# Kernel tuning notes

Hardware: AMD Instinct MI355X
Metric: run time of the kernel (lower is better)

## Reference

```python
import jax, jax.numpy as jnp
import numpy as np

B, C, N, L = 64, 32, 500, 12
C_OUT = 32
C_CAT = 9 * C  # (order*(support_len+1)+1)*c_in = 288


def setup_inputs() -> dict:
    key = jax.random.key(0)
    ks = jax.random.split(key, 7)
    x = jax.random.normal(ks[0], (B, C, N, L), dtype=jnp.float32)
    # row-stochastic-ish adjacencies: scale by 1/N to keep hops numerically tame
    A0 = jax.random.uniform(ks[1], (N, N), dtype=jnp.float32) / N
    A1 = jax.random.uniform(ks[2], (N, N), dtype=jnp.float32) / N
    A2 = jax.random.uniform(ks[3], (N, N), dtype=jnp.float32) / N
    A3 = jax.random.uniform(ks[4], (B, N, N), dtype=jnp.float32) / N
    W = jax.random.normal(ks[5], (C_OUT, C_CAT), dtype=jnp.float32) * 0.05
    b = jax.random.normal(ks[6], (C_OUT,), dtype=jnp.float32) * 0.05
    return {"x": x, "A0": A0, "A1": A1, "A2": A2, "A3": A3, "W": W, "b": b}


def reference(x, A0, A1, A2, A3, W, b):
    # x: [B, C, N, L]; A0..A2: [N, N]; A3: [B, N, N]; W: [C_OUT, 9*C]; b: [C_OUT]
    def hop2(h, A):  # static adjacency
        return jnp.einsum('ncvl,vw->ncwl', h, A)

    def hop3(h, A):  # batched (dynamic) adjacency
        return jnp.einsum('ncvl,nvw->ncwl', h, A)

    out = [x]
    for A in (A0, A1, A2):
        x1 = hop2(x, A)
        x2 = hop2(x1, A)
        out.extend([x1, x2])
    x1 = hop3(x, A3)
    x2 = hop3(x1, A3)
    out.extend([x1, x2])

    h = jnp.concatenate(out, axis=1)  # [B, 9C, N, L]
    # 1x1 Conv2d == channel mixing matmul + bias
    h = jnp.einsum('ncvl,oc->novl', h, W) + b[None, :, None, None]
    # dropout in eval mode: identity
    return h
```

## Files before the change

kernel.cpp:

```cpp
#include <hip/hip_runtime.h>

typedef unsigned short u16;
typedef __bf16 bf16x8 __attribute__((ext_vector_type(8)));
typedef float f32x4 __attribute__((ext_vector_type(4)));
typedef const unsigned int __attribute__((address_space(1))) gu32;
typedef unsigned int __attribute__((address_space(3))) lu32;

#define NN 500
#define LLc 12
#define CC 32
#define MM 384
#define KP 512
#define MT 96
#define NT2 128
#define XS_S 40
#define AS_S 40
#define CT2_S 136
#define TS_S 384
#define AT_ELS 256000

__device__ __forceinline__ u16 f2bf(float f) {
    union { float f; unsigned u; } cv; cv.f = f;
    unsigned u = cv.u;
    u += 0x7fffu + ((u >> 16) & 1u);
    return (u16)(u >> 16);
}
__device__ __forceinline__ float bf2f(u16 s) {
    union { unsigned u; float f; } cv; cv.u = ((unsigned)s) << 16;
    return cv.f;
}

__global__ __launch_bounds__(256) void prep_all(
    const float* __restrict__ x,
    const float* __restrict__ A0, const float* __restrict__ A1,
    const float* __restrict__ A2, const float* __restrict__ A3,
    u16* __restrict__ At_s, u16* __restrict__ At_b,
    u16* __restrict__ Xt,
    const float* __restrict__ W, u16* __restrict__ Wp)
{
    __shared__ u16 Ls[MM * 36];
    const int id = blockIdx.x;
    const int t = threadIdx.x;

    if (id < 17152) {
        int rem = id & 255;
        int z  = id >> 8;
        int n0 = (rem & 15) * 32;
        int k0 = (rem >> 4) * 32;
        const float* Ab; u16* Ob;
        if (z == 0)      { Ab = A0; Ob = At_s; }
        else if (z == 1) { Ab = A1; Ob = At_s + (long)AT_ELS; }
        else if (z == 2) { Ab = A2; Ob = At_s + 2L * AT_ELS; }
        else             { Ab = A3 + (long)(z - 3) * NN * NN; Ob = At_b + (long)(z - 3) * AT_ELS; }
        {
            int vl = t >> 3, u = t & 7;
            float4 v = make_float4(0.f, 0.f, 0.f, 0.f);
            if (k0 + vl < NN && n0 + 4 * u + 4 <= NN)
                v = *(const float4*)(Ab + (long)(k0 + vl) * NN + n0 + 4 * u);
            int nb = 4 * u;
            Ls[(nb + 0) * 36 + vl] = f2bf(v.x);
            Ls[(nb + 1) * 36 + vl] = f2bf(v.y);
            Ls[(nb + 2) * 36 + vl] = f2bf(v.z);
            Ls[(nb + 3) * 36 + vl] = f2bf(v.w);
        }
        __syncthreads();
        {
            int row = t >> 3, u = t & 7;
            if (n0 + row < NN)
                *(uint2*)(Ob + (long)(n0 + row) * KP + k0 + 4 * u) = *(const uint2*)(&Ls[row * 36 + 4 * u]);
        }
    } else if (id < 18176) {
        int jj = id - 17152;
        int v0 = (jj & 15) * 32;
        int b  = jj >> 4;
        #pragma unroll
        for (int j = 0; j < 12; ++j) {
            int f = t + 256 * j;
            int c = f / 96;
            int r = f - c * 96;
            int vl = r / 3;
            int l3 = (r - vl * 3) * 4;
            float4 v = make_float4(0.f, 0.f, 0.f, 0.f);
            if (v0 + vl < NN)
                v = *(const float4*)(x + ((long)b * CC + c) * (NN * LLc) + (long)(v0 + vl) * LLc + l3);
            int mb = (c * LLc + l3) * 36 + vl;
            Ls[mb]       = f2bf(v.x);
            Ls[mb + 36]  = f2bf(v.y);
            Ls[mb + 72]  = f2bf(v.z);
            Ls[mb + 108] = f2bf(v.w);
        }
        __syncthreads();
        #pragma unroll
        for (int j = 0; j < 12; ++j) {
            int f = t + 256 * j;
            int row = f >> 3, u = f & 7;
            *(uint2*)(Xt + ((long)b * MM + row) * KP + v0 + 4 * u) = *(const uint2*)(&Ls[row * 36 + 4 * u]);
        }
    } else {
        int idx = (id - 18176) * 256 + t;
        int j    = idx & 7;
        int lane = (idx >> 3) & 63;
        int p    = (idx >> 9) & 1;
        int mt   = (idx >> 10) & 1;
        int g    = idx >> 11;
        int o  = mt * 16 + (lane & 15);
        int kk = g * 32 + (lane >> 4) * 8 + j;
        float wv = W[o * 288 + kk];
        u16 hi = f2bf(wv);
        Wp[idx] = (p == 0) ? hi : f2bf(wv - bf2f(hi));
    }
}

__global__ __launch_bounds__(256) void atrans_all(
    const float* __restrict__ A0, const float* __restrict__ A1,
    const float* __restrict__ A2, const float* __restrict__ A3,
    u16* __restrict__ At_s, u16* __restrict__ At_b)
{
    __shared__ u16 Ls[32 * 36];
    const int t = threadIdx.x;
    const int n0 = blockIdx.x * 32;
    const int k0 = blockIdx.y * 32;
    const int z = blockIdx.z;
    const float* Ab; u16* Ob;
    if (z == 0)      { Ab = A0; Ob = At_s; }
    else if (z == 1) { Ab = A1; Ob = At_s + (long)AT_ELS; }
    else if (z == 2) { Ab = A2; Ob = At_s + 2L * AT_ELS; }
    else             { Ab = A3 + (long)(z - 3) * NN * NN; Ob = At_b + (long)(z - 3) * AT_ELS; }
    {
        int vl = t >> 3, u = t & 7;
        float4 v = make_float4(0.f, 0.f, 0.f, 0.f);
        if (k0 + vl < NN && n0 + 4 * u + 4 <= NN)
            v = *(const float4*)(Ab + (long)(k0 + vl) * NN + n0 + 4 * u);
        int nb = 4 * u;
        Ls[(nb + 0) * 36 + vl] = f2bf(v.x);
        Ls[(nb + 1) * 36 + vl] = f2bf(v.y);
        Ls[(nb + 2) * 36 + vl] = f2bf(v.z);
        Ls[(nb + 3) * 36 + vl] = f2bf(v.w);
    }
    __syncthreads();
    {
        int row = t >> 3, u = t & 7;
        if (n0 + row < NN)
            *(uint2*)(Ob + (long)(n0 + row) * KP + k0 + 4 * u) = *(const uint2*)(&Ls[row * 36 + 4 * u]);
    }
}

__global__ __launch_bounds__(256) void xpose_kernel(
    const float* __restrict__ x, u16* __restrict__ Xt)
{
    __shared__ u16 Ls[MM * 36];
    const int t = threadIdx.x;
    const int v0 = blockIdx.x * 32;
    const int b  = blockIdx.y;
    #pragma unroll
    for (int j = 0; j < 12; ++j) {
        int f = t + 256 * j;
        int c = f / 96;
        int r = f - c * 96;
        int vl = r / 3;
        int l3 = (r - vl * 3) * 4;
        float4 v = make_float4(0.f, 0.f, 0.f, 0.f);
        if (v0 + vl < NN)
            v = *(const float4*)(x + ((long)b * CC + c) * (NN * LLc) + (long)(v0 + vl) * LLc + l3);
        int mb = (c * LLc + l3) * 36 + vl;
        Ls[mb]       = f2bf(v.x);
        Ls[mb + 36]  = f2bf(v.y);
        Ls[mb + 72]  = f2bf(v.z);
        Ls[mb + 108] = f2bf(v.w);
    }
    __syncthreads();
    #pragma unroll
    for (int j = 0; j < 12; ++j) {
        int f = t + 256 * j;
        int row = f >> 3, u = f & 7;
        *(uint2*)(Xt + ((long)b * MM + row) * KP + v0 + 4 * u) = *(const uint2*)(&Ls[row * 36 + 4 * u]);
    }
}

__global__ __launch_bounds__(256) void wpack_kernel(
    const float* __restrict__ W, u16* __restrict__ Wp)
{
    int idx = blockIdx.x * 256 + threadIdx.x;
    int j    = idx & 7;
    int lane = (idx >> 3) & 63;
    int p    = (idx >> 9) & 1;
    int mt   = (idx >> 10) & 1;
    int g    = idx >> 11;
    int o  = mt * 16 + (lane & 15);
    int kk = g * 32 + (lane >> 4) * 8 + j;
    float wv = W[o * 288 + kk];
    u16 hi = f2bf(wv);
    Wp[idx] = (p == 0) ? hi : f2bf(wv - bf2f(hi));
}

__global__ __launch_bounds__(256, 3) void hop_fast7(
    const u16* __restrict__ Xsrc, long x_gstride, long x_bstride,
    const u16* __restrict__ At_s,
    const u16* __restrict__ At_b,
    u16* __restrict__ Hout, long h_gstride)
{
    __shared__ __align__(16) u16 smem[24576];
    u16* Ct = smem;

    const int t = threadIdx.x;
    const int lane = t & 63;
    const int wv = t >> 6;
    const int f0 = blockIdx.x + 4 * (blockIdx.y + 3 * blockIdx.z);
    const int w  = (f0 & 7) * 384 + (f0 >> 3);
    const int zc = w / 12;
    const int rem = w - zc * 12;
    const int bx = rem & 3;
    const int by = rem >> 2;
    const int g  = zc & 3;
    const int b  = zc >> 2;
    const int n0 = bx * 128;
    const int m0 = by * 128;
    const int ln  = lane & 15;
    const int q16 = lane >> 4;

    const u16* Ab = (g < 3) ? (At_s + (long)g * AT_ELS) : (At_b + (long)b * AT_ELS);
    const u16* Xb = Xsrc + (long)g * x_gstride + (long)b * x_bstride;
    u16* Ob = Hout + (long)g * h_gstride + (long)b * ((long)MM * KP);

    const int rbase = lane >> 2;
    const int coff  = (((lane & 3) ^ ((lane >> 3) & 3)) << 3);
    const int rsel  = ((q16 ^ ((ln >> 1) & 3)) << 3);

    auto STAGE = [&](int kk, int pb) {
        #pragma unroll
        for (int j = 0; j < 4; ++j) {
            int o = (wv * 4 + j) << 10;
            const u16* src;
            if (o < 8192) {
                src = Ab + (long)(n0 + (o >> 6) + rbase) * KP + kk + coff;
            } else {
                src = Xb + (long)(m0 + (o >> 6) - 128 + rbase) * KP + kk + coff;
            }
            __builtin_amdgcn_global_load_lds((gu32*)src,
                (lu32*)((char*)smem + pb * 16384 + o), 16, 0, 0);
        }
    };

    f32x4 acc[2][8];
    #pragma unroll
    for (int ns = 0; ns < 2; ++ns)
        #pragma unroll
        for (int i = 0; i < 8; ++i)
            #pragma unroll
            for (int r = 0; r < 4; ++r) acc[ns][i][r] = 0.f;

    auto COMPUTE = [&](int pb) {
        const u16* As = smem + pb * 8192;
        const u16* Xs = As + 4096;
        bf16x8 b0 = *(const bf16x8*)(&As[(wv * 32 + ln) * 32 + rsel]);
        bf16x8 b1 = *(const bf16x8*)(&As[(wv * 32 + 16 + ln) * 32 + rsel]);
        __builtin_amdgcn_s_setprio(1);
        #pragma unroll
        for (int i = 0; i < 8; ++i) {
            bf16x8 af = *(const bf16x8*)(&Xs[(i * 16 + ln) * 32 + rsel]);
            acc[0][i] = __builtin_amdgcn_mfma_f32_16x16x32_bf16(af, b0, acc[0][i], 0, 0, 0);
            acc[1][i] = __builtin_amdgcn_mfma_f32_16x16x32_bf16(af, b1, acc[1][i], 0, 0, 0);
        }
        __builtin_amdgcn_s_setprio(0);
    };

    STAGE(0, 0);
    STAGE(32, 1);
    int c0 = 0, c1 = 1, c2 = 2;
    #pragma unroll 1
    for (int s = 0; s < 15; ++s) {
        asm volatile("s_waitcnt vmcnt(4)" ::: "memory");
        __builtin_amdgcn_s_barrier();
        __builtin_amdgcn_sched_barrier(0);
        if (s <= 13) STAGE(32 * (s + 2), c2);
        COMPUTE(c0);
        int tmp = c0; c0 = c1; c1 = c2; c2 = tmp;
    }
    asm volatile("s_waitcnt vmcnt(0)" ::: "memory");
    __builtin_amdgcn_s_barrier();
    __builtin_amdgcn_sched_barrier(0);
    COMPUTE(c0);

    #pragma unroll
    for (int h = 0; h < 2; ++h) {
        __syncthreads();
        #pragma unroll
        for (int ns = 0; ns < 2; ++ns) {
            int col = wv * 32 + ns * 16 + ln;
            #pragma unroll
            for (int i4 = 0; i4 < 4; ++i4) {
                int rb = i4 * 16 + (lane >> 4) * 4;
                #pragma unroll
                for (int r = 0; r < 4; ++r)
                    Ct[(rb + r) * CT2_S + col] = f2bf(acc[ns][h * 4 + i4][r]);
            }
        }
        __syncthreads();
        #pragma unroll
        for (int j = 0; j < 8; ++j) {
            int f = t + 256 * j;
            int row = f >> 5, u = f & 31;
            int n = n0 + 4 * u;
            uint2 v = make_uint2(0u, 0u);
            if (n < NN) v = *(const uint2*)(&Ct[row * CT2_S + 4 * u]);
            *(uint2*)(Ob + (long)(m0 + h * 64 + row) * KP + n) = v;
        }
    }
}

__global__ __launch_bounds__(256, 3) void hop_fast3(
    const u16* __restrict__ Xsrc, long x_gstride, long x_bstride, int x_rstride, int x_klim,
    const u16* __restrict__ At_s,
    const u16* __restrict__ At_b,
    u16* __restrict__ Hout, long h_gstride)
{
    __shared__ __align__(16) u16 smem[13056];
    u16* As = smem;
    u16* Xs = smem + 5120;
    u16* Ct = smem;

    const int t = threadIdx.x;
    const int lane = t & 63;
    const int wv = t >> 6;
    const int f0 = blockIdx.x + 4 * blockIdx.y + 8 * blockIdx.z;
    const int w  = (f0 & 7) * 256 + (f0 >> 3);
    const int bx = w & 3;
    const int by = (w >> 2) & 1;
    const int zc = w >> 3;
    const int g  = zc & 3;
    const int b  = zc >> 2;
    const int n0 = bx * NT2;
    const int m0 = by * 192;
    const int ln = lane & 15;
    const int q8 = (lane >> 4) * 8;

    const u16* Ab = (g < 3) ? (At_s + (long)g * AT_ELS) : (At_b + (long)b * AT_ELS);
    const u16* Xb = Xsrc + (long)g * x_gstride + (long)b * x_bstride;
    u16* Ob = Hout + (long)g * h_gstride + (long)b * ((long)MM * NN);

    uint2 pa[4], px[6];
    auto loadA = [&](int k0) {
        #pragma unroll
        for (int j = 0; j < 4; ++j) {
            int f = t + 256 * j;
            int n = f >> 3, u = f & 7;
            uint2 v = make_uint2(0u, 0u);
            if (n0 + n < NN)
                v = *(const uint2*)(Ab + (long)(n0 + n) * KP + k0 + 4 * u);
            pa[j] = v;
        }
    };
    auto loadX = [&](int k0) {
        #pragma unroll
        for (int j = 0; j < 6; ++j) {
            int f = t + 256 * j;
            int r = f >> 3, u = f & 7;
            int k = k0 + 4 * u;
            uint2 v = make_uint2(0u, 0u);
            if (k < x_klim)
                v = *(const uint2*)(Xb + (long)(m0 + r) * x_rstride + k);
            px[j] = v;
        }
    };

    f32x4 acc[2][12];
    #pragma unroll
    for (int ns = 0; ns < 2; ++ns)
        #pragma unroll
        for (int i = 0; i < 12; ++i)
            #pragma unroll
            for (int r = 0; r < 4; ++r) acc[ns][i][r] = 0.f;

    loadA(0);
    loadX(0);
    #pragma unroll 1
    for (int s = 0; s < 16; ++s) {
        __syncthreads();
        #pragma unroll
        for (int j = 0; j < 4; ++j) {
            int f = t + 256 * j;
            *(uint2*)(&As[(f >> 3) * AS_S + 4 * (f & 7)]) = pa[j];
        }
        #pragma unroll
        for (int j = 0; j < 6; ++j) {
            int f = t + 256 * j;
            *(uint2*)(&Xs[(f >> 3) * XS_S + 4 * (f & 7)]) = px[j];
        }
        if (s < 15) {
            loadA(32 * (s + 1));
            loadX(32 * (s + 1));
        }
        __syncthreads();
        bf16x8 b0 = *(const bf16x8*)(&As[(wv * 32 + ln) * AS_S + q8]);
        bf16x8 b1 = *(const bf16x8*)(&As[(wv * 32 + 16 + ln) * AS_S + q8]);
        #pragma unroll
        for (int i = 0; i < 12; ++i) {
            bf16x8 af = *(const bf16x8*)(&Xs[(i * 16 + ln) * XS_S + q8]);
            acc[0][i] = __builtin_amdgcn_mfma_f32_16x16x32_bf16(af, b0, acc[0][i], 0, 0, 0);
            acc[1][i] = __builtin_amdgcn_mfma_f32_16x16x32_bf16(af, b1, acc[1][i], 0, 0, 0);
        }
    }

    #pragma unroll
    for (int h = 0; h < 2; ++h) {
        __syncthreads();
        #pragma unroll
        for (int ns = 0; ns < 2; ++ns) {
            int col = wv * 32 + ns * 16 + ln;
            #pragma unroll
            for (int i6 = 0; i6 < 6; ++i6) {
                int rb = i6 * 16 + (lane >> 4) * 4;
                #pragma unroll
                for (int r = 0; r < 4; ++r)
                    Ct[(rb + r) * CT2_S + col] = f2bf(acc[ns][h * 6 + i6][r]);
            }
        }
        __syncthreads();
        #pragma unroll
        for (int j = 0; j < 12; ++j) {
            int f = t + 256 * j;
            int row = f >> 5, u = f & 31;
            int n = n0 + 4 * u;
            if (n < NN)
                *(uint2*)(Ob + (long)(m0 + h * 96 + row) * NN + n) = *(const uint2*)(&Ct[row * CT2_S + 4 * u]);
        }
    }
}

__global__ __launch_bounds__(512, 4) void mix_mfma(
    const u16* __restrict__ Xt,
    const u16* __restrict__ H,
    const u16* __restrict__ Wp,
    const float* __restrict__ bias,
    float* __restrict__ out,
    long h_gs, long h_bs, int h_rs)
{
    __shared__ __align__(16) char smem[50176];
    u16*   Ls = (u16*)smem;
    float* Ct = (float*)smem;

    const int t   = threadIdx.x;
    const int wg  = blockIdx.y * 8 + blockIdx.x;
    const int swz = (wg & 7) * 64 + (wg >> 3);
    const int bx  = swz & 7;
    const int b   = swz >> 3;
    const int n0  = bx * 64;
    const int w    = t >> 6;
    const int lane = t & 63;
    const int kq   = lane >> 4;
    const int ln   = lane & 15;
    const int srow   = lane >> 3;
    const int schunk = (lane & 7) * 8;

    f32x4 acc[6][2];
    #pragma unroll
    for (int i = 0; i < 6; ++i)
        #pragma unroll
        for (int m = 0; m < 2; ++m)
            #pragma unroll
            for (int r = 0; r < 4; ++r) acc[i][m][r] = 0.f;

    #pragma unroll 1
    for (int g = 0; g < 9; ++g) {
        const u16* base; int rs;
        if (g == 0) { base = Xt + (long)b * (MM * KP); rs = KP; }
        else {
            int gg = g - 1;
            int buf = (gg & 1) ? 4 + (gg >> 1) : (gg >> 1);
            base = H + (long)buf * h_gs + (long)b * h_bs; rs = h_rs;
        }
        __syncthreads();
        #pragma unroll
        for (int i = 0; i < 6; ++i) {
            int r0 = (w * 6 + i) * 8;
            const u16* src = base + (long)(r0 + srow) * rs + n0 + schunk;
            __builtin_amdgcn_global_load_lds((gu32*)src, (lu32*)(Ls + r0 * 64), 16, 0, 0);
        }
        asm volatile("s_waitcnt vmcnt(0)" ::: "memory");
        __syncthreads();
        uint4 wf[2][2];
        #pragma unroll
        for (int mt = 0; mt < 2; ++mt)
            #pragma unroll
            for (int p = 0; p < 2; ++p)
                wf[mt][p] = *(const uint4*)(Wp + ((((g * 2 + mt) * 2 + p) * 64 + lane) * 8));
        #pragma unroll
        for (int i = 0; i < 6; ++i) {
            int ct = w * 6 + i;
            int off0 = kq * 6144 + (ct >> 2) * 64 + (ct & 3) * 16 + ln;
            union { u16 s[8]; bf16x8 v; } fb;
            #pragma unroll
            for (int j = 0; j < 8; ++j) fb.s[j] = Ls[off0 + j * 768];
            #pragma unroll
            for (int mt = 0; mt < 2; ++mt) {
                acc[i][mt] = __builtin_amdgcn_mfma_f32_16x16x32_bf16(*(const bf16x8*)&wf[mt][0], fb.v, acc[i][mt], 0, 0, 0);
                acc[i][mt] = __builtin_amdgcn_mfma_f32_16x16x32_bf16(*(const bf16x8*)&wf[mt][1], fb.v, acc[i][mt], 0, 0, 0);
            }
        }
    }

    #pragma unroll
    for (int mt = 0; mt < 2; ++mt) {
        __syncthreads();
        #pragma unroll
        for (int i = 0; i < 6; ++i) {
            int col = (w * 6 + i) * 16 + ln;
            #pragma unroll
            for (int r = 0; r < 4; ++r)
                Ct[(kq * 4 + r) * 781 + col] = acc[i][mt][r];
        }
        __syncthreads();
        int o16 = t >> 5, u = t & 31;
        int og = mt * 16 + o16;
        float bs = bias[og];
        float* ob = out + (((long)b * CC + og) * NN + n0) * 12L;
        #pragma unroll
        for (int j2 = 0; j2 < 2; ++j2) {
            int n = u + 32 * j2;
            if (n0 + n < NN) {
                float v[12];
                #pragma unroll
                for (int l = 0; l < 12; ++l) v[l] = Ct[o16 * 781 + l * 64 + n] + bs;
                #pragma unroll
                for (int q = 0; q < 3; ++q)
                    *(float4*)(ob + (long)n * 12 + q * 4) = *(const float4*)&v[q * 4];
            }
        }
    }
}

__global__ __launch_bounds__(256, 3) void mix_all(
    const u16* __restrict__ Xt,
    const u16* __restrict__ H,
    const float* __restrict__ W,
    const float* __restrict__ bias,
    float* __restrict__ out)
{
    __shared__ __align__(16) float smem[96 * 36 + 288 * 33];
    float* ts = smem;
    float* Ws = smem + 96 * 36;

    const int t  = threadIdx.x;
    const int b  = blockIdx.y;
    const int w0 = blockIdx.x * 32;
    const int o  = t & 31;
    const int wq = t >> 5;
    const int w4 = wq * 4;
    const long HBUF = (long)64 * MM * NN;

    #pragma unroll
    for (int j = 0; j < 36; ++j) {
        int f = t + 256 * j;
        int oo = f & 31, ci = f >> 5;
        Ws[ci * 33 + oo] = W[oo * 288 + ci];
    }

    float acc[4][12];
    #pragma unroll
    for (int k = 0; k < 4; ++k)
        #pragma unroll
        for (int l = 0; l < 12; ++l) acc[k][l] = 0.f;

    uint2 px[3];
    auto loadq = [&](int q) {
        int g = q >> 2, c0 = (q & 3) << 3;
        const u16* base; int rs;
        if (g == 0) { base = Xt + (long)b * (MM * KP); rs = KP; }
        else {
            int gg = g - 1, i = gg >> 1;
            int buf = (gg & 1) ? 4 + i : i;
            base = H + (long)buf * HBUF + (long)b * ((long)MM * NN); rs = NN;
        }
        int m0c = c0 * 12;
        #pragma unroll
        for (int j = 0; j < 3; ++j) {
            int f = t + 256 * j;
            int r = f >> 3, u = f & 7;
            px[j] = *(const uint2*)(base + (long)(m0c + r) * rs + w0 + 4 * u);
        }
    };

    loadq(0);
    #pragma unroll 1
    for (int q = 0; q < 36; ++q) {
        __syncthreads();
        #pragma unroll
        for (int j = 0; j < 3; ++j) {
            int f = t + 256 * j;
            int r = f >> 3, u = f & 7;
            uint2 raw = px[j];
            float4 v = make_float4(bf2f((u16)(raw.x & 0xffffu)), bf2f((u16)(raw.x >> 16)),
                                   bf2f((u16)(raw.y & 0xffffu)), bf2f((u16)(raw.y >> 16)));
            *(float4*)(&ts[r * 36 + 4 * u]) = v;
        }
        if (q < 35) loadq(q + 1);
        __syncthreads();
        int g = q >> 2, c0 = (q & 3) << 3;
        #pragma unroll 1
        for (int cl = 0; cl < 8; ++cl) {
            float wgt = Ws[(g * 32 + c0 + cl) * 33 + o];
            #pragma unroll
            for (int l = 0; l < 12; ++l) {
                float4 h = *(const float4*)(&ts[(cl * 12 + l) * 36 + w4]);
                acc[0][l] += wgt * h.x;
                acc[1][l] += wgt * h.y;
                acc[2][l] += wgt * h.z;
                acc[3][l] += wgt * h.w;
            }
        }
    }

    #pragma unroll 1
    for (int r = 0; r < 4; ++r) {
        __syncthreads();
        if ((o >> 3) == r) {
            int ol = o & 7;
            #pragma unroll
            for (int k = 0; k < 4; ++k)
                #pragma unroll
                for (int l = 0; l < 12; ++l)
                    ts[ol * 388 + (w4 + k) * 12 + l] = acc[k][l];
        }
        __syncthreads();
        #pragma unroll
        for (int j = 0; j < 3; ++j) {
            int f4 = t + 256 * j;
            int ol = f4 / 96;
            int rem = f4 - ol * 96;
            int w  = rem / 3;
            int lq = rem - w * 3;
            if (w0 + w < NN) {
                float4 v = *(const float4*)(&ts[ol * 388 + w * 12 + lq * 4]);
                float bs = bias[r * 8 + ol];
                v.x += bs; v.y += bs; v.z += bs; v.w += bs;
                *(float4*)(out + (((long)b * CC + r * 8 + ol) * NN + w0 + w) * LLc + lq * 4) = v;
            }
        }
    }
}

__global__ __launch_bounds__(256, 4) void hop_fast(
    const u16* __restrict__ Xsrc, long x_bstride, int x_rstride, int x_klim,
    const u16* __restrict__ At,   long a_bstride,
    u16* __restrict__ hout)
{
    __shared__ __align__(16) u16 smem[13056];
    u16* As = smem;
    u16* Xs = smem + 5120;
    u16* Ct = smem;

    const int t = threadIdx.x;
    const int lane = t & 63;
    const int wv = t >> 6;
    const int n0 = blockIdx.x * NT2;
    const int m0 = blockIdx.y * MT;
    const int b  = blockIdx.z;
    const int ln = lane & 15;
    const int q8 = (lane >> 4) * 8;

    const u16* Ab = At + (long)b * a_bstride;
    const u16* Xb = Xsrc + (long)b * x_bstride;

    uint2 pa[4], px[3];
    auto loadA = [&](int k0) {
        #pragma unroll
        for (int j = 0; j < 4; ++j) {
            int f = t + 256 * j;
            int n = f >> 3, u = f & 7;
            uint2 v = make_uint2(0u, 0u);
            if (n0 + n < NN)
                v = *(const uint2*)(Ab + (long)(n0 + n) * KP + k0 + 4 * u);
            pa[j] = v;
        }
    };
    auto loadX = [&](int k0) {
        #pragma unroll
        for (int j = 0; j < 3; ++j) {
            int f = t + 256 * j;
            int r = f >> 3, u = f & 7;
            int k = k0 + 4 * u;
            uint2 v = make_uint2(0u, 0u);
            if (k < x_klim)
                v = *(const uint2*)(Xb + (long)(m0 + r) * x_rstride + k);
            px[j] = v;
        }
    };

    f32x4 acc[2][6];
    #pragma unroll
    for (int ns = 0; ns < 2; ++ns)
        #pragma unroll
        for (int i = 0; i < 6; ++i)
            #pragma unroll
            for (int r = 0; r < 4; ++r) acc[ns][i][r] = 0.f;

    loadA(0);
    loadX(0);
    #pragma unroll 1
    for (int s = 0; s < 16; ++s) {
        __syncthreads();
        #pragma unroll
        for (int j = 0; j < 4; ++j) {
            int f = t + 256 * j;
            *(uint2*)(&As[(f >> 3) * AS_S + 4 * (f & 7)]) = pa[j];
        }
        #pragma unroll
        for (int j = 0; j < 3; ++j) {
            int f = t + 256 * j;
            *(uint2*)(&Xs[(f >> 3) * XS_S + 4 * (f & 7)]) = px[j];
        }
        if (s < 15) {
            loadA(32 * (s + 1));
            loadX(32 * (s + 1));
        }
        __syncthreads();
        bf16x8 af[6];
        #pragma unroll
        for (int i = 0; i < 6; ++i)
            af[i] = *(const bf16x8*)(&Xs[(i * 16 + ln) * XS_S + q8]);
        #pragma unroll
        for (int ns = 0; ns < 2; ++ns) {
            bf16x8 bfr = *(const bf16x8*)(&As[(wv * 32 + ns * 16 + ln) * AS_S + q8]);
            #pragma unroll
            for (int i = 0; i < 6; ++i)
                acc[ns][i] = __builtin_amdgcn_mfma_f32_16x16x32_bf16(af[i], bfr, acc[ns][i], 0, 0, 0);
        }
    }

    __syncthreads();
    #pragma unroll
    for (int ns = 0; ns < 2; ++ns) {
        int col = wv * 32 + ns * 16 + ln;
        #pragma unroll
        for (int i = 0; i < 6; ++i) {
            int rb = i * 16 + (lane >> 4) * 4;
            #pragma unroll
            for (int r = 0; r < 4; ++r)
                Ct[(rb + r) * CT2_S + col] = f2bf(acc[ns][i][r]);
        }
    }
    __syncthreads();
    u16* Ob = hout + (long)b * ((long)MM * NN);
    #pragma unroll
    for (int j = 0; j < 12; ++j) {
        int f = t + 256 * j;
        int row = f >> 5, u = f & 31;
        int n = n0 + 4 * u;
        if (n < NN)
            *(uint2*)(Ob + (long)(m0 + row) * NN + n) = *(const uint2*)(&Ct[row * CT2_S + 4 * u]);
    }
}

__global__ __launch_bounds__(256, 2) void mix_kernel(
    const float* __restrict__ x,
    const u16* __restrict__ h1,
    const u16* __restrict__ h2,
    const float* __restrict__ W,
    const float* __restrict__ bias,
    int blk1, int blk2,
    float* __restrict__ out, int init)
{
    __shared__ __align__(16) float smem[CC * TS_S + 3 * 1056];
    float* ts = smem;
    float* Ws = smem + CC * TS_S;

    const int t = threadIdx.x;
    const int b = blockIdx.y;
    const int w0 = blockIdx.x * 32;
    const int o  = t & 15;
    const int wg = (t >> 4) & 7;
    const int lh = t >> 7;

    #pragma unroll
    for (int j = 0; j < 4; ++j) {
        int f = t + 256 * j;
        int oo = f & 31, c = f >> 5;
        Ws[c * 33 + oo]        = W[oo * 288 + blk1 * 32 + c];
        Ws[1056 + c * 33 + oo] = W[oo * 288 + blk2 * 32 + c];
        if (init) Ws[2112 + c * 33 + oo] = W[oo * 288 + c];
    }

    float acc2[2][4][6];
    #pragma unroll
    for (int a = 0; a < 2; ++a)
        #pragma unroll
        for (int q = 0; q < 4; ++q)
            #pragma unroll
            for (int l = 0; l < 6; ++l) acc2[a][q][l] = 0.f;

    auto stage_h = [&](const u16* h) {
        #pragma unroll
        for (int j = 0; j < 12; ++j) {
            int f = t + 256 * j;
            int row = f >> 3, u = f & 7;
            int w = w0 + 4 * u;
            uint2 raw = make_uint2(0u, 0u);
            if (w < NN)
                raw = *(const uint2*)(h + ((long)b * MM + row) * NN + w);
            int c = row / 12;
            int l = row - c * 12;
            float* dst = &ts[c * TS_S + l * 32 + 4 * u];
            dst[0] = bf2f((u16)(raw.x & 0xffffu));
            dst[1] = bf2f((u16)(raw.x >> 16));
            dst[2] = bf2f((u16)(raw.y & 0xffffu));
            dst[3] = bf2f((u16)(raw.y >> 16));
        }
    };
    auto accum = [&](const float* Wg) {
        for (int c = 0; c < CC; ++c) {
            float w1 = Wg[c * 33 + o];
            float w2 = Wg[c * 33 + o + 16];
            #pragma unroll
            for (int l6 = 0; l6 < 6; ++l6) {
                const float4 hv = *(const float4*)(&ts[c * TS_S + (lh * 6 + l6) * 32 + wg * 4]);
                acc2[0][0][l6] += w1 * hv.x;
                acc2[0][1][l6] += w1 * hv.y;
                acc2[0][2][l6] += w1 * hv.z;
                acc2[0][3][l6] += w1 * hv.w;
                acc2[1][0][l6] += w2 * hv.x;
                acc2[1][1][l6] += w2 * hv.y;
                acc2[1][2][l6] += w2 * hv.z;
                acc2[1][3][l6] += w2 * hv.w;
            }
        }
    };

    if (init) {
        #pragma unroll
        for (int j = 0; j < 12; ++j) {
            int f = t + 256 * j;
            int c = f / 96;
            int r = f - c * 96;
            int w = r / 3;
            int q = r - w * 3;
            float4 v = make_float4(0.f, 0.f, 0.f, 0.f);
            if (w0 + w < NN)
                v = *(const float4*)(x + ((long)b * CC + c) * (NN * LLc) + (long)(w0 + w) * LLc + q * 4);
            float* dst = &ts[c * TS_S + (q * 4) * 32 + w];
            dst[0]  = v.x; dst[32] = v.y; dst[64] = v.z; dst[96] = v.w;
        }
        __syncthreads();
        accum(Ws + 2112);
        __syncthreads();
    }
    stage_h(h1);
    __syncthreads();
    accum(Ws);
    __syncthreads();
    stage_h(h2);
    __syncthreads();
    accum(Ws + 1056);

    #pragma unroll
    for (int oh = 0; oh < 2; ++oh) {
        int oo = o + 16 * oh;
        float bs = init ? bias[oo] : 0.f;
        #pragma unroll
        for (int q = 0; q < 4; ++q) {
            int w = w0 + wg * 4 + q;
            if (w < NN) {
                float* op = out + ((long)b * CC + oo) * (NN * LLc) + (long)w * LLc + lh * 6;
                #pragma unroll
                for (int p = 0; p < 3; ++p) {
                    float2* pp = (float2*)op + p;
                    float2 v;
                    if (init) {
                        v.x = bs + acc2[oh][q][2 * p];
                        v.y = bs + acc2[oh][q][2 * p + 1];
                    } else {
                        v = *pp;
                        v.x += acc2[oh][q][2 * p];
                        v.y += acc2[oh][q][2 * p + 1];
                    }
                    *pp = v;
                }
            }
        }
    }
}

extern "C" void kernel_launch(void* const* d_in, const int* in_sizes, int n_in,
                              void* d_out, int out_size, void* d_ws, size_t ws_size,
                              hipStream_t stream) {
    const float* x    = (const float*)d_in[0];
    const float* A0   = (const float*)d_in[1];
    const float* A1   = (const float*)d_in[2];
    const float* A2   = (const float*)d_in[3];
    const float* A3   = (const float*)d_in[4];
    const float* W    = (const float*)d_in[5];
    const float* bias = (const float*)d_in[6];
    float* out = (float*)d_out;
    char* ws = (char*)d_ws;

    const size_t HBUF_ELS  = (size_t)64 * MM * NN;
    const size_t H8_BYTES  = 8 * HBUF_ELS * 2;
    const size_t AT_BYTES  = (size_t)AT_ELS * 2;
    const size_t A3T_BYTES = 64 * AT_BYTES;
    const size_t XT_BYTES  = (size_t)64 * MM * KP * 2;
    const size_t need2 = H8_BYTES + 3 * AT_BYTES + A3T_BYTES + XT_BYTES;
    const size_t WPK_BYTES = 36864;
    const size_t need3 = need2 + WPK_BYTES;
    const size_t HB2_ELS  = (size_t)64 * MM * KP;
    const size_t H8B_PAD  = 8 * HB2_ELS * 2;
    const size_t need4 = H8B_PAD + 3 * AT_BYTES + A3T_BYTES + XT_BYTES + WPK_BYTES;

    dim3 blk(256);

    if (ws_size >= need4) {
        u16* Hb   = (u16*)ws;
        u16* At_s = (u16*)(ws + H8B_PAD);
        u16* A3t  = At_s + 3L * AT_ELS;
        u16* Xt   = (u16*)(ws + H8B_PAD + 3 * AT_BYTES + A3T_BYTES);
        u16* Wpk  = Xt + (size_t)64 * MM * KP;

        prep_all<<<dim3(18248), blk, 0, stream>>>(x, A0, A1, A2, A3, At_s, A3t, Xt, W, Wpk);
        hop_fast7<<<dim3(4, 3, 256), blk, 0, stream>>>(
            Xt, 0L, (long)MM * KP, At_s, A3t, Hb, (long)HB2_ELS);
        hop_fast7<<<dim3(4, 3, 256), blk, 0, stream>>>(
            Hb, (long)HB2_ELS, (long)MM * KP, At_s, A3t,
            Hb + 4 * HB2_ELS, (long)HB2_ELS);
        mix_mfma<<<dim3(8, 64), dim3(512), 0, stream>>>(
            Xt, Hb, Wpk, bias, out, (long)HB2_ELS, (long)MM * KP, KP);
        return;
    }

    dim3 hgrid(4, 2, 256);

    if (ws_size >= need3) {
        u16* Hb   = (u16*)ws;
        u16* At_s = (u16*)(ws + H8_BYTES);
        u16* A3t  = At_s + 3L * AT_ELS;
        u16* Xt   = (u16*)(ws + H8_BYTES + 3 * AT_BYTES + A3T_BYTES);
        u16* Wpk  = (u16*)(ws + need2);

        atrans_all<<<dim3(16, 16, 67), blk, 0, stream>>>(A0, A1, A2, A3, At_s, A3t);
        xpose_kernel<<<dim3(16, 64), blk, 0, stream>>>(x, Xt);
        wpack_kernel<<<dim3(72), blk, 0, stream>>>(W, Wpk);
        hop_fast3<<<hgrid, blk, 0, stream>>>(
            Xt, 0L, (long)MM * KP, KP, KP, At_s, A3t, Hb, (long)HBUF_ELS);
        hop_fast3<<<hgrid, blk, 0, stream>>>(
            Hb, (long)HBUF_ELS, (long)MM * NN, NN, NN, At_s, A3t,
            Hb + 4 * HBUF_ELS, (long)HBUF_ELS);
        mix_mfma<<<dim3(8, 64), dim3(512), 0, stream>>>(
            Xt, Hb, Wpk, bias, out, (long)HBUF_ELS, (long)MM * NN, NN);
        return;
    }

    if (ws_size >= need2) {
        u16* H    = (u16*)ws;
        u16* At_s = (u16*)(ws + H8_BYTES);
        u16* A3t  = At_s + 3L * AT_ELS;
        u16* Xt   = (u16*)(ws + H8_BYTES + 3 * AT_BYTES + A3T_BYTES);

        atrans_all<<<dim3(16, 16, 67), blk, 0, stream>>>(A0, A1, A2, A3, At_s, A3t);
        xpose_kernel<<<dim3(16, 64), blk, 0, stream>>>(x, Xt);
        hop_fast3<<<hgrid, blk, 0, stream>>>(
            Xt, 0L, (long)MM * KP, KP, KP, At_s, A3t, H, (long)HBUF_ELS);
        hop_fast3<<<hgrid, blk, 0, stream>>>(
            H, (long)HBUF_ELS, (long)MM * NN, NN, NN, At_s, A3t,
            H + 4 * HBUF_ELS, (long)HBUF_ELS);
        mix_all<<<dim3(16, 64), blk, 0, stream>>>(Xt, H, W, bias, out);
        return;
    }

    const size_t H_BYTES   = HBUF_ELS * 2;
    const size_t need_at   = 2 * H_BYTES + 3 * AT_BYTES + A3T_BYTES;

    u16* H1 = (u16*)ws;
    u16* H2 = (u16*)(ws + H_BYTES);
    u16* At0 = (u16*)(ws + 2 * H_BYTES);
    u16* A3t = At0 + 3L * AT_ELS;
    u16* Xt  = (u16*)(ws + need_at);

    dim3 fgrid(4, 4, 64);
    dim3 mgrid(16, 64);

    xpose_kernel<<<dim3(16, 64), blk, 0, stream>>>(x, Xt);
    atrans_all<<<dim3(16, 16, 67), blk, 0, stream>>>(A0, A1, A2, A3, At0, A3t);

    const long XT_BS = (long)MM * KP;
    const long H_BS  = (long)MM * NN;
    u16* Atp[4] = {At0, At0 + (long)AT_ELS, At0 + 2L * AT_ELS, A3t};

    for (int i = 0; i < 4; ++i) {
        long a_bs = (i == 3) ? (long)AT_ELS : 0;
        hop_fast<<<fgrid, blk, 0, stream>>>(Xt, XT_BS, KP, KP, Atp[i], a_bs, H1);
        hop_fast<<<fgrid, blk, 0, stream>>>(H1, H_BS, NN, NN, Atp[i], a_bs, H2);
        mix_kernel<<<mgrid, blk, 0, stream>>>(i == 0 ? x : nullptr, H1, H2, W, bias,
                                              2 * i + 1, 2 * i + 2, out, i == 0 ? 1 : 0);
    }
}
```

Before: 364.4 us.

## Emit hop outputs in mix-friendly channel-contiguous layout and stream mix from global

Adds a new path in which the hop kernels write their results twice: in the existing K-major layout for the second hop, and in an (l, n, c)-contiguous layout grouped by 8 channels that the mix kernel can read directly as MFMA B fragments. The hop tile changes to 96 rows (8 channels × 12 timesteps) so each block owns whole channel groups. The second hop skips the K-major write entirely. mix_stream drops LDS staging and the scalar gather transposes, loading 16-byte fragments straight from global. The cost is extra writes and workspace in the first hop, and a different hop tiling.

Measured after the change: 365.7 us. About the same (+0.4%).

```diff
diff --git a/kernel.cpp b/kernel.cpp
--- a/kernel.cpp
+++ b/kernel.cpp
@@ -18,6 +18,10 @@
 #define CT2_S 136
 #define TS_S 384
 #define AT_ELS 256000
+#define HM_G 12288000L
+#define HM_B 192000L
+#define HCL_G 12582912L
+#define HCL_B 196608L
 
 __device__ __forceinline__ u16 f2bf(float f) {
     union { float f; unsigned u; } cv; cv.f = f;
@@ -35,7 +39,7 @@
     const float* __restrict__ A0, const float* __restrict__ A1,
     const float* __restrict__ A2, const float* __restrict__ A3,
     u16* __restrict__ At_s, u16* __restrict__ At_b,
-    u16* __restrict__ Xt,
+    u16* __restrict__ Xt, u16* __restrict__ Xm,
     const float* __restrict__ W, u16* __restrict__ Wp)
 {
     __shared__ u16 Ls[MM * 36];
@@ -96,6 +100,24 @@
             int row = f >> 3, u = f & 7;
             *(uint2*)(Xt + ((long)b * MM + row) * KP + v0 + 4 * u) = *(const uint2*)(&Ls[row * 36 + 4 * u]);
         }
+        if (Xm) {
+            u16* Xb = Xm + (long)b * HM_B;
+            #pragma unroll
+            for (int j = 0; j < 6; ++j) {
+                int f = t + 256 * j;
+                int vl = f & 31;
+                int lq = f >> 5;
+                int l  = lq % 12;
+                int cq = lq / 12;
+                if (v0 + vl < NN) {
+                    union { u16 s[8]; uint4 v; } pk;
+                    #pragma unroll
+                    for (int c8 = 0; c8 < 8; ++c8)
+                        pk.s[c8] = Ls[((cq * 8 + c8) * 12 + l) * 36 + vl];
+                    *(uint4*)(Xb + ((long)(l * NN + v0 + vl)) * 32 + cq * 8) = pk.v;
+                }
+            }
+        }
     } else {
         int idx = (id - 18176) * 256 + t;
         int j    = idx & 7;
@@ -108,6 +130,446 @@
         float wv = W[o * 288 + kk];
         u16 hi = f2bf(wv);
         Wp[idx] = (p == 0) ? hi : f2bf(wv - bf2f(hi));
+    }
+}
+
+__global__ __launch_bounds__(256, 3) void hop_fast8(
+    const u16* __restrict__ Xsrc, long x_gstride, long x_bstride,
+    const u16* __restrict__ At_s,
+    const u16* __restrict__ At_b,
+    u16* __restrict__ Hcl,
+    u16* __restrict__ HmArg)
+{
+    __shared__ __align__(16) u16 smem[21504];
+    u16* Ct = smem;
+
+    const int t = threadIdx.x;
+    const int lane = t & 63;
+    const int wv = t >> 6;
+    const int f0 = blockIdx.x + 4 * (blockIdx.y + 4 * blockIdx.z);
+    const int w  = (f0 & 7) * 2048 + (f0 >> 3);
+    const int zc = w >> 4;
+    const int rem = w & 15;
+    const int bx = rem & 3;
+    const int my = rem >> 2;
+    const int g  = zc & 3;
+    const int b  = zc >> 2;
+    const int n0 = bx * NT2;
+    const int m0 = my * 96;
+    const int cb = my * 8;
+    const int ln  = lane & 15;
+    const int q16 = lane >> 4;
+
+    const u16* Ab = (g < 3) ? (At_s + (long)g * AT_ELS) : (At_b + (long)b * AT_ELS);
+    const u16* Xb = Xsrc + (long)g * x_gstride + (long)b * x_bstride;
+
+    const int rbase = lane >> 2;
+    const int coff  = (((lane & 3) ^ ((lane >> 3) & 3)) << 3);
+    const int rsel  = ((q16 ^ ((ln >> 1) & 3)) << 3);
+
+    auto STAGE = [&](int kk, int pb) {
+        char* base = (char*)smem + pb * 14336;
+        if (wv < 2) {
+            #pragma unroll
+            for (int j = 0; j < 4; ++j) {
+                int r16 = wv * 4 + j;
+                const u16* src = Ab + (long)(n0 + r16 * 16 + rbase) * KP + kk + coff;
+                __builtin_amdgcn_global_load_lds((gu32*)src, (lu32*)(base + r16 * 1024), 16, 0, 0);
+            }
+        } else {
+            #pragma unroll
+            for (int j = 0; j < 3; ++j) {
+                int r16 = (wv - 2) * 3 + j;
+                const u16* src = Xb + (long)(m0 + r16 * 16 + rbase) * KP + kk + coff;
+                __builtin_amdgcn_global_load_lds((gu32*)src, (lu32*)(base + 8192 + r16 * 1024), 16, 0, 0);
+            }
+        }
+    };
+
+    f32x4 acc[2][6];
+    #pragma unroll
+    for (int ns = 0; ns < 2; ++ns)
+        #pragma unroll
+        for (int i = 0; i < 6; ++i)
+            #pragma unroll
+            for (int r = 0; r < 4; ++r) acc[ns][i][r] = 0.f;
+
+    auto COMPUTE = [&](int pb) {
+        const u16* As = smem + pb * 7168;
+        const u16* Xs = As + 4096;
+        bf16x8 b0 = *(const bf16x8*)(&As[(wv * 32 + ln) * 32 + rsel]);
+        bf16x8 b1 = *(const bf16x8*)(&As[(wv * 32 + 16 + ln) * 32 + rsel]);
+        __builtin_amdgcn_s_setprio(1);
+        #pragma unroll
+        for (int i = 0; i < 6; ++i) {
+            bf16x8 af = *(const bf16x8*)(&Xs[(i * 16 + ln) * 32 + rsel]);
+            acc[0][i] = __builtin_amdgcn_mfma_f32_16x16x32_bf16(af, b0, acc[0][i], 0, 0, 0);
+            acc[1][i] = __builtin_amdgcn_mfma_f32_16x16x32_bf16(af, b1, acc[1][i], 0, 0, 0);
+        }
+        __builtin_amdgcn_s_setprio(0);
+    };
+
+    STAGE(0, 0);
+    STAGE(32, 1);
+    int c0 = 0, c1 = 1, c2 = 2;
+    #pragma unroll 1
+    for (int s = 0; s < 15; ++s) {
+        if (wv < 2) asm volatile("s_waitcnt vmcnt(4)" ::: "memory");
+        else        asm volatile("s_waitcnt vmcnt(3)" ::: "memory");
+        __builtin_amdgcn_s_barrier();
+        __builtin_amdgcn_sched_barrier(0);
+        if (s <= 13) STAGE(32 * (s + 2), c2);
+        COMPUTE(c0);
+        int tmp = c0; c0 = c1; c1 = c2; c2 = tmp;
+    }
+    asm volatile("s_waitcnt vmcnt(0)" ::: "memory");
+    __builtin_amdgcn_s_barrier();
+    __builtin_amdgcn_sched_barrier(0);
+    COMPUTE(c0);
+
+    __syncthreads();
+    #pragma unroll
+    for (int ns = 0; ns < 2; ++ns) {
+        int col = wv * 32 + ns * 16 + ln;
+        #pragma unroll
+        for (int i6 = 0; i6 < 6; ++i6) {
+            int rb = i6 * 16 + (lane >> 4) * 4;
+            #pragma unroll
+            for (int r = 0; r < 4; ++r)
+                Ct[(rb + r) * CT2_S + col] = f2bf(acc[ns][i6][r]);
+        }
+    }
+    __syncthreads();
+    if (Hcl) {
+        u16* Ocl = Hcl + (long)g * HCL_G + (long)b * HCL_B;
+        #pragma unroll
+        for (int j = 0; j < 12; ++j) {
+            int f = t + 256 * j;
+            int row = f >> 5, u = f & 31;
+            int n = n0 + 4 * u;
+            uint2 v = make_uint2(0u, 0u);
+            if (n < NN) v = *(const uint2*)(&Ct[row * CT2_S + 4 * u]);
+            *(uint2*)(Ocl + (long)(m0 + row) * KP + n) = v;
+        }
+    }
+    {
+        u16* Om = HmArg + (long)g * HM_G + (long)b * HM_B;
+        #pragma unroll
+        for (int j = 0; j < 6; ++j) {
+            int f = t + 256 * j;
+            int n_l = f & 127;
+            int l   = f >> 7;
+            int n = n0 + n_l;
+            if (n < NN) {
+                union { u16 s[8]; uint4 v; } pk;
+                #pragma unroll
+                for (int c8 = 0; c8 < 8; ++c8)
+                    pk.s[c8] = Ct[(c8 * 12 + l) * CT2_S + n_l];
+                *(uint4*)(Om + ((long)(l * NN + n)) * 32 + cb) = pk.v;
+            }
+        }
+    }
+}
+
+__global__ __launch_bounds__(256, 3) void hop_fast7(
+    const u16* __restrict__ Xsrc, long x_gstride, long x_bstride,
+    const u16* __restrict__ At_s,
+    const u16* __restrict__ At_b,
+    u16* __restrict__ Hout, long h_gstride)
+{
+    __shared__ __align__(16) u16 smem[24576];
+    u16* Ct = smem;
+
+    const int t = threadIdx.x;
+    const int lane = t & 63;
+    const int wv = t >> 6;
+    const int f0 = blockIdx.x + 4 * (blockIdx.y + 3 * blockIdx.z);
+    const int w  = (f0 & 7) * 384 + (f0 >> 3);
+    const int zc = w / 12;
+    const int rem = w - zc * 12;
+    const int bx = rem & 3;
+    const int by = rem >> 2;
+    const int g  = zc & 3;
+    const int b  = zc >> 2;
+    const int n0 = bx * 128;
+    const int m0 = by * 128;
+    const int ln  = lane & 15;
+    const int q16 = lane >> 4;
+
+    const u16* Ab = (g < 3) ? (At_s + (long)g * AT_ELS) : (At_b + (long)b * AT_ELS);
+    const u16* Xb = Xsrc + (long)g * x_gstride + (long)b * x_bstride;
+    u16* Ob = Hout + (long)g * h_gstride + (long)b * ((long)MM * KP);
+
+    const int rbase = lane >> 2;
+    const int coff  = (((lane & 3) ^ ((lane >> 3) & 3)) << 3);
+    const int rsel  = ((q16 ^ ((ln >> 1) & 3)) << 3);
+
+    auto STAGE = [&](int kk, int pb) {
+        #pragma unroll
+        for (int j = 0; j < 4; ++j) {
+            int o = (wv * 4 + j) << 10;
+            const u16* src;
+            if (o < 8192) src = Ab + (long)(n0 + (o >> 6) + rbase) * KP + kk + coff;
+            else          src = Xb + (long)(m0 + (o >> 6) - 128 + rbase) * KP + kk + coff;
+            __builtin_amdgcn_global_load_lds((gu32*)src,
+                (lu32*)((char*)smem + pb * 16384 + o), 16, 0, 0);
+        }
+    };
+
+    f32x4 acc[2][8];
+    #pragma unroll
+    for (int ns = 0; ns < 2; ++ns)
+        #pragma unroll
+        for (int i = 0; i < 8; ++i)
+            #pragma unroll
+            for (int r = 0; r < 4; ++r) acc[ns][i][r] = 0.f;
+
+    auto COMPUTE = [&](int pb) {
+        const u16* As = smem + pb * 8192;
+        const u16* Xs = As + 4096;
+        bf16x8 b0 = *(const bf16x8*)(&As[(wv * 32 + ln) * 32 + rsel]);
+        bf16x8 b1 = *(const bf16x8*)(&As[(wv * 32 + 16 + ln) * 32 + rsel]);
+        __builtin_amdgcn_s_setprio(1);
+        #pragma unroll
+        for (int i = 0; i < 8; ++i) {
+            bf16x8 af = *(const bf16x8*)(&Xs[(i * 16 + ln) * 32 + rsel]);
+            acc[0][i] = __builtin_amdgcn_mfma_f32_16x16x32_bf16(af, b0, acc[0][i], 0, 0, 0);
+            acc[1][i] = __builtin_amdgcn_mfma_f32_16x16x32_bf16(af, b1, acc[1][i], 0, 0, 0);
+        }
+        __builtin_amdgcn_s_setprio(0);
+    };
+
+    STAGE(0, 0);
+    STAGE(32, 1);
+    int c0 = 0, c1 = 1, c2 = 2;
+    #pragma unroll 1
+    for (int s = 0; s < 15; ++s) {
+        asm volatile("s_waitcnt vmcnt(4)" ::: "memory");
+        __builtin_amdgcn_s_barrier();
+        __builtin_amdgcn_sched_barrier(0);
+        if (s <= 13) STAGE(32 * (s + 2), c2);
+        COMPUTE(c0);
+        int tmp = c0; c0 = c1; c1 = c2; c2 = tmp;
+    }
+    asm volatile("s_waitcnt vmcnt(0)" ::: "memory");
+    __builtin_amdgcn_s_barrier();
+    __builtin_amdgcn_sched_barrier(0);
+    COMPUTE(c0);
+
+    #pragma unroll
+    for (int h = 0; h < 2; ++h) {
+        __syncthreads();
+        #pragma unroll
+        for (int ns = 0; ns < 2; ++ns) {
+            int col = wv * 32 + ns * 16 + ln;
+            #pragma unroll
+            for (int i4 = 0; i4 < 4; ++i4) {
+                int rb = i4 * 16 + (lane >> 4) * 4;
+                #pragma unroll
+                for (int r = 0; r < 4; ++r)
+                    Ct[(rb + r) * CT2_S + col] = f2bf(acc[ns][h * 4 + i4][r]);
+            }
+        }
+        __syncthreads();
+        #pragma unroll
+        for (int j = 0; j < 8; ++j) {
+            int f = t + 256 * j;
+            int row = f >> 5, u = f & 31;
+            int n = n0 + 4 * u;
+            uint2 v = make_uint2(0u, 0u);
+            if (n < NN) v = *(const uint2*)(&Ct[row * CT2_S + 4 * u]);
+            *(uint2*)(Ob + (long)(m0 + h * 64 + row) * KP + n) = v;
+        }
+    }
+}
+
+__global__ __launch_bounds__(512, 4) void mix_stream(
+    const u16* __restrict__ Xm,
+    const u16* __restrict__ Hm,
+    const u16* __restrict__ Wp,
+    const float* __restrict__ bias,
+    float* __restrict__ out)
+{
+    __shared__ __align__(16) float Ct[12496];
+
+    const int t   = threadIdx.x;
+    const int wg  = blockIdx.y * 8 + blockIdx.x;
+    const int swz = (wg & 7) * 64 + (wg >> 3);
+    const int bx  = swz & 7;
+    const int b   = swz >> 3;
+    const int n0  = bx * 64;
+    const int w    = t >> 6;
+    const int lane = t & 63;
+    const int kq   = lane >> 4;
+    const int ln   = lane & 15;
+
+    f32x4 acc[6][2];
+    #pragma unroll
+    for (int i = 0; i < 6; ++i)
+        #pragma unroll
+        for (int m = 0; m < 2; ++m)
+            #pragma unroll
+            for (int r = 0; r < 4; ++r) acc[i][m][r] = 0.f;
+
+    #pragma unroll 1
+    for (int g = 0; g < 9; ++g) {
+        const u16* src;
+        if (g == 0) src = Xm + (long)b * HM_B;
+        else {
+            int gg = g - 1;
+            int buf = (gg & 1) ? 4 + (gg >> 1) : (gg >> 1);
+            src = Hm + (long)buf * HM_G + (long)b * HM_B;
+        }
+        uint4 wf[2][2];
+        #pragma unroll
+        for (int mt = 0; mt < 2; ++mt)
+            #pragma unroll
+            for (int p = 0; p < 2; ++p)
+                wf[mt][p] = *(const uint4*)(Wp + ((((g * 2 + mt) * 2 + p) * 64 + lane) * 8));
+        #pragma unroll
+        for (int i = 0; i < 6; ++i) {
+            int ct = w * 6 + i;
+            int l  = ct >> 2;
+            int n  = n0 + ((ct & 3) << 4) + ln;
+            uint4 fbv = make_uint4(0u, 0u, 0u, 0u);
+            if (n < NN) fbv = *(const uint4*)(src + ((long)(l * NN + n)) * 32 + kq * 8);
+            bf16x8 fb = *(const bf16x8*)&fbv;
+            acc[i][0] = __builtin_amdgcn_mfma_f32_16x16x32_bf16(*(const bf16x8*)&wf[0][0], fb, acc[i][0], 0, 0, 0);
+            acc[i][0] = __builtin_amdgcn_mfma_f32_16x16x32_bf16(*(const bf16x8*)&wf[0][1], fb, acc[i][0], 0, 0, 0);
+            acc[i][1] = __builtin_amdgcn_mfma_f32_16x16x32_bf16(*(const bf16x8*)&wf[1][0], fb, acc[i][1], 0, 0, 0);
+            acc[i][1] = __builtin_amdgcn_mfma_f32_16x16x32_bf16(*(const bf16x8*)&wf[1][1], fb, acc[i][1], 0, 0, 0);
+        }
+    }
+
+    #pragma unroll
+    for (int mt = 0; mt < 2; ++mt) {
+        __syncthreads();
+        #pragma unroll
+        for (int i = 0; i < 6; ++i) {
+            int col = (w * 6 + i) * 16 + ln;
+            #pragma unroll
+            for (int r = 0; r < 4; ++r)
+                Ct[(kq * 4 + r) * 781 + col] = acc[i][mt][r];
+        }
+        __syncthreads();
+        int o16 = t >> 5, u = t & 31;
+        int og = mt * 16 + o16;
+        float bs = bias[og];
+        float* ob = out + (((long)b * CC + og) * NN + n0) * 12L;
+        #pragma unroll
+        for (int j2 = 0; j2 < 2; ++j2) {
+            int n = u + 32 * j2;
+            if (n0 + n < NN) {
+                float v[12];
+                #pragma unroll
+                for (int l = 0; l < 12; ++l) v[l] = Ct[o16 * 781 + l * 64 + n] + bs;
+                #pragma unroll
+                for (int q = 0; q < 3; ++q)
+                    *(float4*)(ob + (long)n * 12 + q * 4) = *(const float4*)&v[q * 4];
+            }
+        }
+    }
+}
+
+__global__ __launch_bounds__(512, 4) void mix_mfma(
+    const u16* __restrict__ Xt,
+    const u16* __restrict__ H,
+    const u16* __restrict__ Wp,
+    const float* __restrict__ bias,
+    float* __restrict__ out,
+    long h_gs, long h_bs, int h_rs)
+{
+    __shared__ __align__(16) char smem[50176];
+    u16*   Ls = (u16*)smem;
+    float* Ct = (float*)smem;
+
+    const int t   = threadIdx.x;
+    const int wg  = blockIdx.y * 8 + blockIdx.x;
+    const int swz = (wg & 7) * 64 + (wg >> 3);
+    const int bx  = swz & 7;
+    const int b   = swz >> 3;
+    const int n0  = bx * 64;
+    const int w    = t >> 6;
+    const int lane = t & 63;
+    const int kq   = lane >> 4;
+    const int ln   = lane & 15;
+    const int srow   = lane >> 3;
+    const int schunk = (lane & 7) * 8;
+
+    f32x4 acc[6][2];
+    #pragma unroll
+    for (int i = 0; i < 6; ++i)
+        #pragma unroll
+        for (int m = 0; m < 2; ++m)
+            #pragma unroll
+            for (int r = 0; r < 4; ++r) acc[i][m][r] = 0.f;
+
+    #pragma unroll 1
+    for (int g = 0; g < 9; ++g) {
+        const u16* base; int rs;
+        if (g == 0) { base = Xt + (long)b * (MM * KP); rs = KP; }
+        else {
+            int gg = g - 1;
+            int buf = (gg & 1) ? 4 + (gg >> 1) : (gg >> 1);
+            base = H + (long)buf * h_gs + (long)b * h_bs; rs = h_rs;
+        }
+        __syncthreads();
+        #pragma unroll
+        for (int i = 0; i < 6; ++i) {
+            int r0 = (w * 6 + i) * 8;
+            const u16* src = base + (long)(r0 + srow) * rs + n0 + schunk;
+            __builtin_amdgcn_global_load_lds((gu32*)src, (lu32*)(Ls + r0 * 64), 16, 0, 0);
+        }
+        asm volatile("s_waitcnt vmcnt(0)" ::: "memory");
+        __syncthreads();
+        uint4 wf[2][2];
+        #pragma unroll
+        for (int mt = 0; mt < 2; ++mt)
+            #pragma unroll
+            for (int p = 0; p < 2; ++p)
+                wf[mt][p] = *(const uint4*)(Wp + ((((g * 2 + mt) * 2 + p) * 64 + lane) * 8));
+        #pragma unroll
+        for (int i = 0; i < 6; ++i) {
+            int ct = w * 6 + i;
+            int off0 = kq * 6144 + (ct >> 2) * 64 + (ct & 3) * 16 + ln;
+            union { u16 s[8]; bf16x8 v; } fb;
+            #pragma unroll
+            for (int j = 0; j < 8; ++j) fb.s[j] = Ls[off0 + j * 768];
+            #pragma unroll
+            for (int mt = 0; mt < 2; ++mt) {
+                acc[i][mt] = __builtin_amdgcn_mfma_f32_16x16x32_bf16(*(const bf16x8*)&wf[mt][0], fb.v, acc[i][mt], 0, 0, 0);
+                acc[i][mt] = __builtin_amdgcn_mfma_f32_16x16x32_bf16(*(const bf16x8*)&wf[mt][1], fb.v, acc[i][mt], 0, 0, 0);
+            }
+        }
+    }
+
+    #pragma unroll
+    for (int mt = 0; mt < 2; ++mt) {
+        __syncthreads();
+        #pragma unroll
+        for (int i = 0; i < 6; ++i) {
+            int col = (w * 6 + i) * 16 + ln;
+            #pragma unroll
+            for (int r = 0; r < 4; ++r)
+                Ct[(kq * 4 + r) * 781 + col] = acc[i][mt][r];
+        }
+        __syncthreads();
+        int o16 = t >> 5, u = t & 31;
+        int og = mt * 16 + o16;
+        float bs = bias[og];
+        float* ob = out + (((long)b * CC + og) * NN + n0) * 12L;
+        #pragma unroll
+        for (int j2 = 0; j2 < 2; ++j2) {
+            int n = u + 32 * j2;
+            if (n0 + n < NN) {
+                float v[12];
+                #pragma unroll
+                for (int l = 0; l < 12; ++l) v[l] = Ct[o16 * 781 + l * 64 + n] + bs;
+                #pragma unroll
+                for (int q = 0; q < 3; ++q)
+                    *(float4*)(ob + (long)n * 12 + q * 4) = *(const float4*)&v[q * 4];
+            }
+        }
     }
 }
 
@@ -177,468 +639,6 @@
     }
 }
 
-__global__ __launch_bounds__(256) void wpack_kernel(
-    const float* __restrict__ W, u16* __restrict__ Wp)
-{
-    int idx = blockIdx.x * 256 + threadIdx.x;
-    int j    = idx & 7;
-    int lane = (idx >> 3) & 63;
-    int p    = (idx >> 9) & 1;
-    int mt   = (idx >> 10) & 1;
-    int g    = idx >> 11;
-    int o  = mt * 16 + (lane & 15);
-    int kk = g * 32 + (lane >> 4) * 8 + j;
-    float wv = W[o * 288 + kk];
-    u16 hi = f2bf(wv);
-    Wp[idx] = (p == 0) ? hi : f2bf(wv - bf2f(hi));
-}
-
-__global__ __launch_bounds__(256, 3) void hop_fast7(
-    const u16* __restrict__ Xsrc, long x_gstride, long x_bstride,
-    const u16* __restrict__ At_s,
-    const u16* __restrict__ At_b,
-    u16* __restrict__ Hout, long h_gstride)
-{
-    __shared__ __align__(16) u16 smem[24576];
-    u16* Ct = smem;
-
-    const int t = threadIdx.x;
-    const int lane = t & 63;
-    const int wv = t >> 6;
-    const int f0 = blockIdx.x + 4 * (blockIdx.y + 3 * blockIdx.z);
-    const int w  = (f0 & 7) * 384 + (f0 >> 3);
-    const int zc = w / 12;
-    const int rem = w - zc * 12;
-    const int bx = rem & 3;
-    const int by = rem >> 2;
-    const int g  = zc & 3;
-    const int b  = zc >> 2;
-    const int n0 = bx * 128;
-    const int m0 = by * 128;
-    const int ln  = lane & 15;
-    const int q16 = lane >> 4;
-
-    const u16* Ab = (g < 3) ? (At_s + (long)g * AT_ELS) : (At_b + (long)b * AT_ELS);
-    const u16* Xb = Xsrc + (long)g * x_gstride + (long)b * x_bstride;
-    u16* Ob = Hout + (long)g * h_gstride + (long)b * ((long)MM * KP);
-
-    const int rbase = lane >> 2;
-    const int coff  = (((lane & 3) ^ ((lane >> 3) & 3)) << 3);
-    const int rsel  = ((q16 ^ ((ln >> 1) & 3)) << 3);
-
-    auto STAGE = [&](int kk, int pb) {
-        #pragma unroll
-        for (int j = 0; j < 4; ++j) {
-            int o = (wv * 4 + j) << 10;
-            const u16* src;
-            if (o < 8192) {
-                src = Ab + (long)(n0 + (o >> 6) + rbase) * KP + kk + coff;
-            } else {
-                src = Xb + (long)(m0 + (o >> 6) - 128 + rbase) * KP + kk + coff;
-            }
-            __builtin_amdgcn_global_load_lds((gu32*)src,
-                (lu32*)((char*)smem + pb * 16384 + o), 16, 0, 0);
-        }
-    };
-
-    f32x4 acc[2][8];
-    #pragma unroll
-    for (int ns = 0; ns < 2; ++ns)
-        #pragma unroll
-        for (int i = 0; i < 8; ++i)
-            #pragma unroll
-            for (int r = 0; r < 4; ++r) acc[ns][i][r] = 0.f;
-
-    auto COMPUTE = [&](int pb) {
-        const u16* As = smem + pb * 8192;
-        const u16* Xs = As + 4096;
-        bf16x8 b0 = *(const bf16x8*)(&As[(wv * 32 + ln) * 32 + rsel]);
-        bf16x8 b1 = *(const bf16x8*)(&As[(wv * 32 + 16 + ln) * 32 + rsel]);
-        __builtin_amdgcn_s_setprio(1);
-        #pragma unroll
-        for (int i = 0; i < 8; ++i) {
-            bf16x8 af = *(const bf16x8*)(&Xs[(i * 16 + ln) * 32 + rsel]);
-            acc[0][i] = __builtin_amdgcn_mfma_f32_16x16x32_bf16(af, b0, acc[0][i], 0, 0, 0);
-            acc[1][i] = __builtin_amdgcn_mfma_f32_16x16x32_bf16(af, b1, acc[1][i], 0, 0, 0);
-        }
-        __builtin_amdgcn_s_setprio(0);
-    };
-
-    STAGE(0, 0);
-    STAGE(32, 1);
-    int c0 = 0, c1 = 1, c2 = 2;
-    #pragma unroll 1
-    for (int s = 0; s < 15; ++s) {
-        asm volatile("s_waitcnt vmcnt(4)" ::: "memory");
-        __builtin_amdgcn_s_barrier();
-        __builtin_amdgcn_sched_barrier(0);
-        if (s <= 13) STAGE(32 * (s + 2), c2);
-        COMPUTE(c0);
-        int tmp = c0; c0 = c1; c1 = c2; c2 = tmp;
-    }
-    asm volatile("s_waitcnt vmcnt(0)" ::: "memory");
-    __builtin_amdgcn_s_barrier();
-    __builtin_amdgcn_sched_barrier(0);
-    COMPUTE(c0);
-
-    #pragma unroll
-    for (int h = 0; h < 2; ++h) {
-        __syncthreads();
-        #pragma unroll
-        for (int ns = 0; ns < 2; ++ns) {
-            int col = wv * 32 + ns * 16 + ln;
-            #pragma unroll
-            for (int i4 = 0; i4 < 4; ++i4) {
-                int rb = i4 * 16 + (lane >> 4) * 4;
-                #pragma unroll
-                for (int r = 0; r < 4; ++r)
-                    Ct[(rb + r) * CT2_S + col] = f2bf(acc[ns][h * 4 + i4][r]);
-            }
-        }
-        __syncthreads();
-        #pragma unroll
-        for (int j = 0; j < 8; ++j) {
-            int f = t + 256 * j;
-            int row = f >> 5, u = f & 31;
-            int n = n0 + 4 * u;
-            uint2 v = make_uint2(0u, 0u);
-            if (n < NN) v = *(const uint2*)(&Ct[row * CT2_S + 4 * u]);
-            *(uint2*)(Ob + (long)(m0 + h * 64 + row) * KP + n) = v;
-        }
-    }
-}
-
-__global__ __launch_bounds__(256, 3) void hop_fast3(
-    const u16* __restrict__ Xsrc, long x_gstride, long x_bstride, int x_rstride, int x_klim,
-    const u16* __restrict__ At_s,
-    const u16* __restrict__ At_b,
-    u16* __restrict__ Hout, long h_gstride)
-{
-    __shared__ __align__(16) u16 smem[13056];
-    u16* As = smem;
-    u16* Xs = smem + 5120;
-    u16* Ct = smem;
-
-    const int t = threadIdx.x;
-    const int lane = t & 63;
-    const int wv = t >> 6;
-    const int f0 = blockIdx.x + 4 * blockIdx.y + 8 * blockIdx.z;
-    const int w  = (f0 & 7) * 256 + (f0 >> 3);
-    const int bx = w & 3;
-    const int by = (w >> 2) & 1;
-    const int zc = w >> 3;
-    const int g  = zc & 3;
-    const int b  = zc >> 2;
-    const int n0 = bx * NT2;
-    const int m0 = by * 192;
-    const int ln = lane & 15;
-    const int q8 = (lane >> 4) * 8;
-
-    const u16* Ab = (g < 3) ? (At_s + (long)g * AT_ELS) : (At_b + (long)b * AT_ELS);
-    const u16* Xb = Xsrc + (long)g * x_gstride + (long)b * x_bstride;
-    u16* Ob = Hout + (long)g * h_gstride + (long)b * ((long)MM * NN);
-
-    uint2 pa[4], px[6];
-    auto loadA = [&](int k0) {
-        #pragma unroll
-        for (int j = 0; j < 4; ++j) {
-            int f = t + 256 * j;
-            int n = f >> 3, u = f & 7;
-            uint2 v = make_uint2(0u, 0u);
-            if (n0 + n < NN)
-                v = *(const uint2*)(Ab + (long)(n0 + n) * KP + k0 + 4 * u);
-            pa[j] = v;
-        }
-    };
-    auto loadX = [&](int k0) {
-        #pragma unroll
-        for (int j = 0; j < 6; ++j) {
-            int f = t + 256 * j;
-            int r = f >> 3, u = f & 7;
-            int k = k0 + 4 * u;
-            uint2 v = make_uint2(0u, 0u);
-            if (k < x_klim)
-                v = *(const uint2*)(Xb + (long)(m0 + r) * x_rstride + k);
-            px[j] = v;
-        }
-    };
-
-    f32x4 acc[2][12];
-    #pragma unroll
-    for (int ns = 0; ns < 2; ++ns)
-        #pragma unroll
-        for (int i = 0; i < 12; ++i)
-            #pragma unroll
-            for (int r = 0; r < 4; ++r) acc[ns][i][r] = 0.f;
-
-    loadA(0);
-    loadX(0);
-    #pragma unroll 1
-    for (int s = 0; s < 16; ++s) {
-        __syncthreads();
-        #pragma unroll
-        for (int j = 0; j < 4; ++j) {
-            int f = t + 256 * j;
-            *(uint2*)(&As[(f >> 3) * AS_S + 4 * (f & 7)]) = pa[j];
-        }
-        #pragma unroll
-        for (int j = 0; j < 6; ++j) {
-            int f = t + 256 * j;
-            *(uint2*)(&Xs[(f >> 3) * XS_S + 4 * (f & 7)]) = px[j];
-        }
-        if (s < 15) {
-            loadA(32 * (s + 1));
-            loadX(32 * (s + 1));
-        }
-        __syncthreads();
-        bf16x8 b0 = *(const bf16x8*)(&As[(wv * 32 + ln) * AS_S + q8]);
-        bf16x8 b1 = *(const bf16x8*)(&As[(wv * 32 + 16 + ln) * AS_S + q8]);
-        #pragma unroll
-        for (int i = 0; i < 12; ++i) {
-            bf16x8 af = *(const bf16x8*)(&Xs[(i * 16 + ln) * XS_S + q8]);
-            acc[0][i] = __builtin_amdgcn_mfma_f32_16x16x32_bf16(af, b0, acc[0][i], 0, 0, 0);
-            acc[1][i] = __builtin_amdgcn_mfma_f32_16x16x32_bf16(af, b1, acc[1][i], 0, 0, 0);
-        }
-    }
-
-    #pragma unroll
-    for (int h = 0; h < 2; ++h) {
-        __syncthreads();
-        #pragma unroll
-        for (int ns = 0; ns < 2; ++ns) {
-            int col = wv * 32 + ns * 16 + ln;
-            #pragma unroll
-            for (int i6 = 0; i6 < 6; ++i6) {
-                int rb = i6 * 16 + (lane >> 4) * 4;
-                #pragma unroll
-                for (int r = 0; r < 4; ++r)
-                    Ct[(rb + r) * CT2_S + col] = f2bf(acc[ns][h * 6 + i6][r]);
-            }
-        }
-        __syncthreads();
-        #pragma unroll
-        for (int j = 0; j < 12; ++j) {
-            int f = t + 256 * j;
-            int row = f >> 5, u = f & 31;
-            int n = n0 + 4 * u;
-            if (n < NN)
-                *(uint2*)(Ob + (long)(m0 + h * 96 + row) * NN + n) = *(const uint2*)(&Ct[row * CT2_S + 4 * u]);
-        }
-    }
-}
-
-__global__ __launch_bounds__(512, 4) void mix_mfma(
-    const u16* __restrict__ Xt,
-    const u16* __restrict__ H,
-    const u16* __restrict__ Wp,
-    const float* __restrict__ bias,
-    float* __restrict__ out,
-    long h_gs, long h_bs, int h_rs)
-{
-    __shared__ __align__(16) char smem[50176];
-    u16*   Ls = (u16*)smem;
-    float* Ct = (float*)smem;
-
-    const int t   = threadIdx.x;
-    const int wg  = blockIdx.y * 8 + blockIdx.x;
-    const int swz = (wg & 7) * 64 + (wg >> 3);
-    const int bx  = swz & 7;
-    const int b   = swz >> 3;
-    const int n0  = bx * 64;
-    const int w    = t >> 6;
-    const int lane = t & 63;
-    const int kq   = lane >> 4;
-    const int ln   = lane & 15;
-    const int srow   = lane >> 3;
-    const int schunk = (lane & 7) * 8;
-
-    f32x4 acc[6][2];
-    #pragma unroll
-    for (int i = 0; i < 6; ++i)
-        #pragma unroll
-        for (int m = 0; m < 2; ++m)
-            #pragma unroll
-            for (int r = 0; r < 4; ++r) acc[i][m][r] = 0.f;
-
-    #pragma unroll 1
-    for (int g = 0; g < 9; ++g) {
-        const u16* base; int rs;
-        if (g == 0) { base = Xt + (long)b * (MM * KP); rs = KP; }
-        else {
-            int gg = g - 1;
-            int buf = (gg & 1) ? 4 + (gg >> 1) : (gg >> 1);
-            base = H + (long)buf * h_gs + (long)b * h_bs; rs = h_rs;
-        }
-        __syncthreads();
-        #pragma unroll
-        for (int i = 0; i < 6; ++i) {
-            int r0 = (w * 6 + i) * 8;
-            const u16* src = base + (long)(r0 + srow) * rs + n0 + schunk;
-            __builtin_amdgcn_global_load_lds((gu32*)src, (lu32*)(Ls + r0 * 64), 16, 0, 0);
-        }
-        asm volatile("s_waitcnt vmcnt(0)" ::: "memory");
-        __syncthreads();
-        uint4 wf[2][2];
-        #pragma unroll
-        for (int mt = 0; mt < 2; ++mt)
-            #pragma unroll
-            for (int p = 0; p < 2; ++p)
-                wf[mt][p] = *(const uint4*)(Wp + ((((g * 2 + mt) * 2 + p) * 64 + lane) * 8));
-        #pragma unroll
-        for (int i = 0; i < 6; ++i) {
-            int ct = w * 6 + i;
-            int off0 = kq * 6144 + (ct >> 2) * 64 + (ct & 3) * 16 + ln;
-            union { u16 s[8]; bf16x8 v; } fb;
-            #pragma unroll
-            for (int j = 0; j < 8; ++j) fb.s[j] = Ls[off0 + j * 768];
-            #pragma unroll
-            for (int mt = 0; mt < 2; ++mt) {
-                acc[i][mt] = __builtin_amdgcn_mfma_f32_16x16x32_bf16(*(const bf16x8*)&wf[mt][0], fb.v, acc[i][mt], 0, 0, 0);
-                acc[i][mt] = __builtin_amdgcn_mfma_f32_16x16x32_bf16(*(const bf16x8*)&wf[mt][1], fb.v, acc[i][mt], 0, 0, 0);
-            }
-        }
-    }
-
-    #pragma unroll
-    for (int mt = 0; mt < 2; ++mt) {
-        __syncthreads();
-        #pragma unroll
-        for (int i = 0; i < 6; ++i) {
-            int col = (w * 6 + i) * 16 + ln;
-            #pragma unroll
-            for (int r = 0; r < 4; ++r)
-                Ct[(kq * 4 + r) * 781 + col] = acc[i][mt][r];
-        }
-        __syncthreads();
-        int o16 = t >> 5, u = t & 31;
-        int og = mt * 16 + o16;
-        float bs = bias[og];
-        float* ob = out + (((long)b * CC + og) * NN + n0) * 12L;
-        #pragma unroll
-        for (int j2 = 0; j2 < 2; ++j2) {
-            int n = u + 32 * j2;
-            if (n0 + n < NN) {
-                float v[12];
-                #pragma unroll
-                for (int l = 0; l < 12; ++l) v[l] = Ct[o16 * 781 + l * 64 + n] + bs;
-                #pragma unroll
-                for (int q = 0; q < 3; ++q)
-                    *(float4*)(ob + (long)n * 12 + q * 4) = *(const float4*)&v[q * 4];
-            }
-        }
-    }
-}
-
-__global__ __launch_bounds__(256, 3) void mix_all(
-    const u16* __restrict__ Xt,
-    const u16* __restrict__ H,
-    const float* __restrict__ W,
-    const float* __restrict__ bias,
-    float* __restrict__ out)
-{
-    __shared__ __align__(16) float smem[96 * 36 + 288 * 33];
-    float* ts = smem;
-    float* Ws = smem + 96 * 36;
-
-    const int t  = threadIdx.x;
-    const int b  = blockIdx.y;
-    const int w0 = blockIdx.x * 32;
-    const int o  = t & 31;
-    const int wq = t >> 5;
-    const int w4 = wq * 4;
-    const long HBUF = (long)64 * MM * NN;
-
-    #pragma unroll
-    for (int j = 0; j < 36; ++j) {
-        int f = t + 256 * j;
-        int oo = f & 31, ci = f >> 5;
-        Ws[ci * 33 + oo] = W[oo * 288 + ci];
-    }
-
-    float acc[4][12];
-    #pragma unroll
-    for (int k = 0; k < 4; ++k)
-        #pragma unroll
-        for (int l = 0; l < 12; ++l) acc[k][l] = 0.f;
-
-    uint2 px[3];
-    auto loadq = [&](int q) {
-        int g = q >> 2, c0 = (q & 3) << 3;
-        const u16* base; int rs;
-        if (g == 0) { base = Xt + (long)b * (MM * KP); rs = KP; }
-        else {
-            int gg = g - 1, i = gg >> 1;
-            int buf = (gg & 1) ? 4 + i : i;
-            base = H + (long)buf * HBUF + (long)b * ((long)MM * NN); rs = NN;
-        }
-        int m0c = c0 * 12;
-        #pragma unroll
-        for (int j = 0; j < 3; ++j) {
-            int f = t + 256 * j;
-            int r = f >> 3, u = f & 7;
-            px[j] = *(const uint2*)(base + (long)(m0c + r) * rs + w0 + 4 * u);
-        }
-    };
-
-    loadq(0);
-    #pragma unroll 1
-    for (int q = 0; q < 36; ++q) {
-        __syncthreads();
-        #pragma unroll
-        for (int j = 0; j < 3; ++j) {
-            int f = t + 256 * j;
-            int r = f >> 3, u = f & 7;
-            uint2 raw = px[j];
-            float4 v = make_float4(bf2f((u16)(raw.x & 0xffffu)), bf2f((u16)(raw.x >> 16)),
-                                   bf2f((u16)(raw.y & 0xffffu)), bf2f((u16)(raw.y >> 16)));
-            *(float4*)(&ts[r * 36 + 4 * u]) = v;
-        }
-        if (q < 35) loadq(q + 1);
-        __syncthreads();
-        int g = q >> 2, c0 = (q & 3) << 3;
-        #pragma unroll 1
-        for (int cl = 0; cl < 8; ++cl) {
-            float wgt = Ws[(g * 32 + c0 + cl) * 33 + o];
-            #pragma unroll
-            for (int l = 0; l < 12; ++l) {
-                float4 h = *(const float4*)(&ts[(cl * 12 + l) * 36 + w4]);
-                acc[0][l] += wgt * h.x;
-                acc[1][l] += wgt * h.y;
-                acc[2][l] += wgt * h.z;
-                acc[3][l] += wgt * h.w;
-            }
-        }
-    }
-
-    #pragma unroll 1
-    for (int r = 0; r < 4; ++r) {
-        __syncthreads();
-        if ((o >> 3) == r) {
-            int ol = o & 7;
-            #pragma unroll
-            for (int k = 0; k < 4; ++k)
-                #pragma unroll
-                for (int l = 0; l < 12; ++l)
-                    ts[ol * 388 + (w4 + k) * 12 + l] = acc[k][l];
-        }
-        __syncthreads();
-        #pragma unroll
-        for (int j = 0; j < 3; ++j) {
-            int f4 = t + 256 * j;
-            int ol = f4 / 96;
-            int rem = f4 - ol * 96;
-            int w  = rem / 3;
-            int lq = rem - w * 3;
-            if (w0 + w < NN) {
-                float4 v = *(const float4*)(&ts[ol * 388 + w * 12 + lq * 4]);
-                float bs = bias[r * 8 + ol];
-                v.x += bs; v.y += bs; v.z += bs; v.w += bs;
-                *(float4*)(out + (((long)b * CC + r * 8 + ol) * NN + w0 + w) * LLc + lq * 4) = v;
-            }
-        }
-    }
-}
-
 __global__ __launch_bounds__(256, 4) void hop_fast(
     const u16* __restrict__ Xsrc, long x_bstride, int x_rstride, int x_klim,
     const u16* __restrict__ At,   long a_bstride,
@@ -892,19 +892,39 @@
     float* out = (float*)d_out;
     char* ws = (char*)d_ws;
 
-    const size_t HBUF_ELS  = (size_t)64 * MM * NN;
-    const size_t H8_BYTES  = 8 * HBUF_ELS * 2;
     const size_t AT_BYTES  = (size_t)AT_ELS * 2;
     const size_t A3T_BYTES = 64 * AT_BYTES;
     const size_t XT_BYTES  = (size_t)64 * MM * KP * 2;
-    const size_t need2 = H8_BYTES + 3 * AT_BYTES + A3T_BYTES + XT_BYTES;
     const size_t WPK_BYTES = 36864;
-    const size_t need3 = need2 + WPK_BYTES;
-    const size_t HB2_ELS  = (size_t)64 * MM * KP;
-    const size_t H8B_PAD  = 8 * HB2_ELS * 2;
+    const size_t HB2_ELS   = (size_t)64 * MM * KP;
+    const size_t H8B_PAD   = 8 * HB2_ELS * 2;
     const size_t need4 = H8B_PAD + 3 * AT_BYTES + A3T_BYTES + XT_BYTES + WPK_BYTES;
 
+    const size_t HCL_BYTES = 4 * HB2_ELS * 2;
+    const size_t HM_BYTES  = 8 * (size_t)HM_G * 2;
+    const size_t XM_BYTES  = 64 * (size_t)HM_B * 2;
+    const size_t need5 = HCL_BYTES + HM_BYTES + 3 * AT_BYTES + A3T_BYTES
+                       + XT_BYTES + XM_BYTES + WPK_BYTES;
+
     dim3 blk(256);
+
+    if (ws_size >= need5) {
+        u16* Hcl  = (u16*)ws;
+        u16* Hm   = (u16*)(ws + HCL_BYTES);
+        u16* At_s = (u16*)(ws + HCL_BYTES + HM_BYTES);
+        u16* A3t  = At_s + 3L * AT_ELS;
+        u16* Xt   = (u16*)((char*)A3t + A3T_BYTES);
+        u16* Xm   = Xt + (size_t)64 * MM * KP;
+        u16* Wpk  = Xm + 64 * (size_t)HM_B;
+
+        prep_all<<<dim3(18248), blk, 0, stream>>>(x, A0, A1, A2, A3, At_s, A3t, Xt, Xm, W, Wpk);
+        hop_fast8<<<dim3(4, 4, 1024), blk, 0, stream>>>(
+            Xt, 0L, (long)MM * KP, At_s, A3t, Hcl, Hm);
+        hop_fast8<<<dim3(4, 4, 1024), blk, 0, stream>>>(
+            Hcl, (long)HCL_G, (long)HCL_B, At_s, A3t, (u16*)nullptr, Hm + 4 * HM_G);
+        mix_stream<<<dim3(8, 64), dim3(512), 0, stream>>>(Xm, Hm, Wpk, bias, out);
+        return;
+    }
 
     if (ws_size >= need4) {
         u16* Hb   = (u16*)ws;
@@ -913,7 +933,7 @@
         u16* Xt   = (u16*)(ws + H8B_PAD + 3 * AT_BYTES + A3T_BYTES);
         u16* Wpk  = Xt + (size_t)64 * MM * KP;
 
-        prep_all<<<dim3(18248), blk, 0, stream>>>(x, A0, A1, A2, A3, At_s, A3t, Xt, W, Wpk);
+        prep_all<<<dim3(18248), blk, 0, stream>>>(x, A0, A1, A2, A3, At_s, A3t, Xt, (u16*)nullptr, W, Wpk);
         hop_fast7<<<dim3(4, 3, 256), blk, 0, stream>>>(
             Xt, 0L, (long)MM * KP, At_s, A3t, Hb, (long)HB2_ELS);
         hop_fast7<<<dim3(4, 3, 256), blk, 0, stream>>>(
@@ -924,45 +944,7 @@
         return;
     }
 
-    dim3 hgrid(4, 2, 256);
-
-    if (ws_size >= need3) {
-        u16* Hb   = (u16*)ws;
-        u16* At_s = (u16*)(ws + H8_BYTES);
-        u16* A3t  = At_s + 3L * AT_ELS;
-        u16* Xt   = (u16*)(ws + H8_BYTES + 3 * AT_BYTES + A3T_BYTES);
-        u16* Wpk  = (u16*)(ws + need2);
-
-        atrans_all<<<dim3(16, 16, 67), blk, 0, stream>>>(A0, A1, A2, A3, At_s, A3t);
-        xpose_kernel<<<dim3(16, 64), blk, 0, stream>>>(x, Xt);
-        wpack_kernel<<<dim3(72), blk, 0, stream>>>(W, Wpk);
-        hop_fast3<<<hgrid, blk, 0, stream>>>(
-            Xt, 0L, (long)MM * KP, KP, KP, At_s, A3t, Hb, (long)HBUF_ELS);
-        hop_fast3<<<hgrid, blk, 0, stream>>>(
-            Hb, (long)HBUF_ELS, (long)MM * NN, NN, NN, At_s, A3t,
-            Hb + 4 * HBUF_ELS, (long)HBUF_ELS);
-        mix_mfma<<<dim3(8, 64), dim3(512), 0, stream>>>(
-            Xt, Hb, Wpk, bias, out, (long)HBUF_ELS, (long)MM * NN, NN);
-        return;
-    }
-
-    if (ws_size >= need2) {
-        u16* H    = (u16*)ws;
-        u16* At_s = (u16*)(ws + H8_BYTES);
-        u16* A3t  = At_s + 3L * AT_ELS;
-        u16* Xt   = (u16*)(ws + H8_BYTES + 3 * AT_BYTES + A3T_BYTES);
-
-        atrans_all<<<dim3(16, 16, 67), blk, 0, stream>>>(A0, A1, A2, A3, At_s, A3t);
-        xpose_kernel<<<dim3(16, 64), blk, 0, stream>>>(x, Xt);
-        hop_fast3<<<hgrid, blk, 0, stream>>>(
-            Xt, 0L, (long)MM * KP, KP, KP, At_s, A3t, H, (long)HBUF_ELS);
-        hop_fast3<<<hgrid, blk, 0, stream>>>(
-            H, (long)HBUF_ELS, (long)MM * NN, NN, NN, At_s, A3t,
-            H + 4 * HBUF_ELS, (long)HBUF_ELS);
-        mix_all<<<dim3(16, 64), blk, 0, stream>>>(Xt, H, W, bias, out);
-        return;
-    }
-
+    const size_t HBUF_ELS  = (size_t)64 * MM * NN;
     const size_t H_BYTES   = HBUF_ELS * 2;
     const size_t need_at   = 2 * H_BYTES + 3 * AT_BYTES + A3T_BYTES;
 
```
